# Kernel tuning notes

Hardware: AMD Instinct MI355X
Metric: run time of the kernel (lower is better)

The kernel has to match this reference:

```python
import jax, jax.numpy as jnp
import numpy as np

EMBED_DIM = 1024
NUM_HEADS = 16
HEAD_DIM = EMBED_DIM // NUM_HEADS


def setup_inputs() -> dict:
    key = jax.random.key(0)
    k_x, k_qkv, k_w, k_b = jax.random.split(key, 4)
    B, N, C = 2, 2048, EMBED_DIM
    scale = 1.0 / np.sqrt(C)
    x = jax.random.normal(k_x, (B, N, C), dtype=jnp.float32)
    # nn.Linear(embed_dim, 3*embed_dim, bias=False): weight [3C, C]
    w_qkv = jax.random.normal(k_qkv, (3 * C, C), dtype=jnp.float32) * scale
    # nn.Linear(embed_dim, embed_dim): weight [C, C], bias [C]
    w_out = jax.random.normal(k_w, (C, C), dtype=jnp.float32) * scale
    b_out = jax.random.normal(k_b, (C,), dtype=jnp.float32) * scale
    return {"x": x, "w_qkv": w_qkv, "w_out": w_out, "b_out": b_out}


def reference(x, w_qkv, w_out, b_out):
    B, N, C = x.shape
    H, D = NUM_HEADS, HEAD_DIM
    # qkv projection: [B,N,3C] -> [3,B,H,N,D]
    qkv = jnp.einsum("bnc,fc->bnf", x, w_qkv)
    qkv = qkv.reshape(B, N, 3, H, D).transpose(2, 0, 3, 1, 4)
    q, k, v = qkv[0], qkv[1], qkv[2]
    # scaled dot-product attention (dropout p=0 / eval mode -> identity)
    scores = jnp.einsum("bhnd,bhmd->bhnm", q, k) / np.sqrt(D).astype(x.dtype)
    attn = jax.nn.softmax(scores, axis=-1)
    out = jnp.einsum("bhnm,bhmd->bhnd", attn, v)
    out = out.transpose(0, 2, 1, 3).reshape(B, N, C)
    return jnp.einsum("bnc,oc->bno", out, w_out) + b_out
```

## Files before the change

### kernel.cpp

```cpp
#include <hip/hip_runtime.h>
#include <hip/hip_bf16.h>

typedef unsigned short u16;
typedef __attribute__((ext_vector_type(4))) float f32x4;
typedef __attribute__((ext_vector_type(8))) short bf16x8;

#define MFMA16(a, b, c) __builtin_amdgcn_mfma_f32_16x16x32_bf16(a, b, c, 0, 0, 0)

__device__ __forceinline__ u16 f2bf(float f) {
    union { float f; unsigned u; } v;
    v.f = f;
    unsigned r = v.u + 0x7FFFu + ((v.u >> 16) & 1u);
    return (u16)(r >> 16);
}

__device__ __forceinline__ int4 pack8(const float4 a, const float4 b) {
    int4 r;
    r.x = (int)((unsigned)f2bf(a.x) | ((unsigned)f2bf(a.y) << 16));
    r.y = (int)((unsigned)f2bf(a.z) | ((unsigned)f2bf(a.w) << 16));
    r.z = (int)((unsigned)f2bf(b.x) | ((unsigned)f2bf(b.y) << 16));
    r.w = (int)((unsigned)f2bf(b.z) | ((unsigned)f2bf(b.w) << 16));
    return r;
}

__device__ __forceinline__ unsigned pk2(float a, float b) {
    __hip_bfloat162 t = __float22bfloat162_rn(make_float2(a, b));
    union { __hip_bfloat162 h; unsigned u; } c;
    c.h = t;
    return c.u;
}

__device__ __forceinline__ void gload_lds16(const u16* g, u16* l) {
    __builtin_amdgcn_global_load_lds(
        (const __attribute__((address_space(1))) void*)g,
        (__attribute__((address_space(3))) void*)l, 16, 0, 0);
}

__global__ __launch_bounds__(256) void cvt_kernel(
    const float* __restrict__ x, const float* __restrict__ wq,
    const float* __restrict__ wo, u16* __restrict__ outb)
{
    size_t i = ((size_t)blockIdx.x * 256 + threadIdx.x) * 8;
    const float* src;
    size_t off;
    if (i < 4194304)      { src = x;  off = i; }
    else if (i < 7340032) { src = wq; off = i - 4194304; }
    else                  { src = wo; off = i - 7340032; }
    float4 a = *(const float4*)(src + off);
    float4 b = *(const float4*)(src + off + 4);
    *(int4*)(outb + i) = pack8(a, b);
}

__global__ __launch_bounds__(512) void qkv_gemm_kernel(
    const u16* __restrict__ X, const u16* __restrict__ W,
    u16* __restrict__ qws, u16* __restrict__ kws, u16* __restrict__ vws)
{
    __shared__ __align__(16) u16 Ash[256 * 64];
    __shared__ __align__(16) u16 Bsh[128 * 64];
    const int id = blockIdx.x;
    const int xcd = id & 7, slot = id >> 3;
    const int bm = (xcd >> 1) * 4 + (slot & 3);
    const int bn = (xcd & 1) * 12 + (slot >> 2);
    const int tid = threadIdx.x;
    const int lane = tid & 63, wid = tid >> 6;
    const int wm = wid >> 1, wn = wid & 1;
    const int g = lane >> 4, lq = lane & 15;

    f32x4 acc[4][4];
#pragma unroll
    for (int i = 0; i < 4; i++)
#pragma unroll
        for (int j = 0; j < 4; j++) acc[i][j] = (f32x4){0.f, 0.f, 0.f, 0.f};

    const int lrow = lane >> 3;
    const int lchunk = (lane & 7) ^ lrow;
    const u16* Ab = X + (size_t)(bm * 256 + lrow) * 1024 + lchunk * 8;
    const u16* Bb = W + (size_t)(bn * 128 + lrow) * 1024 + lchunk * 8;

    for (int kt = 0; kt < 16; ++kt) {
#pragma unroll
        for (int i = 0; i < 4; i++) {
            int sub = wid * 4 + i;
            gload_lds16(Ab + (size_t)sub * 8192 + kt * 64, &Ash[sub * 512]);
        }
#pragma unroll
        for (int i = 0; i < 2; i++) {
            int sub = wid * 2 + i;
            gload_lds16(Bb + (size_t)sub * 8192 + kt * 64, &Bsh[sub * 512]);
        }
        __syncthreads();
#pragma unroll
        for (int ka = 0; ka < 2; ka++) {
            bf16x8 af[4], bfr[4];
#pragma unroll
            for (int mt = 0; mt < 4; mt++) {
                int row = wm * 64 + mt * 16 + lq;
                af[mt] = *(const bf16x8*)&Ash[row * 64 + (((ka * 4 + g) ^ (row & 7)) << 3)];
            }
#pragma unroll
            for (int nt = 0; nt < 4; nt++) {
                int row = wn * 64 + nt * 16 + lq;
                bfr[nt] = *(const bf16x8*)&Bsh[row * 64 + (((ka * 4 + g) ^ (row & 7)) << 3)];
            }
#pragma unroll
            for (int mt = 0; mt < 4; mt++)
#pragma unroll
                for (int nt = 0; nt < 4; nt++)
                    acc[mt][nt] = MFMA16(af[mt], bfr[nt], acc[mt][nt]);
        }
        __syncthreads();
    }

#pragma unroll
    for (int mt = 0; mt < 4; mt++) {
#pragma unroll
        for (int nt = 0; nt < 4; nt++) {
            int f = bn * 128 + wn * 64 + nt * 16 + lq;
            int t = f >> 10, h = (f >> 6) & 15, d = f & 63;
            int mbase = bm * 256 + wm * 64 + mt * 16 + g * 4;
            int b = mbase >> 11, n0 = mbase & 2047;
            if (t == 0) {
#pragma unroll
                for (int r = 0; r < 4; r++)
                    qws[((size_t)(b * 16 + h) * 2048 + n0 + r) * 64 + d] =
                        f2bf(acc[mt][nt][r] * 0.18033688f);
            } else if (t == 1) {
#pragma unroll
                for (int r = 0; r < 4; r++)
                    kws[((size_t)(b * 16 + h) * 2048 + n0 + r) * 64 + d] =
                        f2bf(acc[mt][nt][r]);
            } else {
                ushort4 pk;
                pk.x = f2bf(acc[mt][nt][0]);
                pk.y = f2bf(acc[mt][nt][1]);
                pk.z = f2bf(acc[mt][nt][2]);
                pk.w = f2bf(acc[mt][nt][3]);
                *(ushort4*)&vws[((size_t)(b * 16 + h) * 64 + d) * 2048 + n0] = pk;
            }
        }
    }
}

__global__ __launch_bounds__(256, 2) void attn_kernel(
    const u16* __restrict__ qws, const u16* __restrict__ kws,
    const u16* __restrict__ vws, float* __restrict__ Opart,
    float* __restrict__ lpart)
{
    __shared__ __align__(16) u16 Ksh[2][64 * 64];
    __shared__ __align__(16) u16 Vsh[2][64 * 64];
    __shared__ __align__(16) u16 Psh[4][64 * 64];
    const int bh = blockIdx.x, qt = blockIdx.y, kvh = blockIdx.z;
    const int tid = threadIdx.x, wid = tid >> 6, lane = tid & 63;
    const int g = lane >> 4, lq = lane & 15;

    const u16* Qp = qws + ((size_t)bh * 2048 + qt * 256 + wid * 64) * 64;
    bf16x8 qf[4][2];
#pragma unroll
    for (int qa = 0; qa < 4; qa++) {
        qf[qa][0] = *(const bf16x8*)(Qp + (qa * 16 + lq) * 64 + g * 8);
        qf[qa][1] = *(const bf16x8*)(Qp + (qa * 16 + lq) * 64 + 32 + g * 8);
    }

    const int lrow = lane >> 3;
    const int lchunk = (lane & 7) ^ lrow;
    const u16* Kb = kws + (size_t)bh * 2048 * 64 + (size_t)lrow * 64 + lchunk * 8;
    const u16* Vb = vws + (size_t)bh * 64 * 2048 + (size_t)lrow * 2048 + lchunk * 8;

#define STAGE(TG, BUF)                                                        \
    {                                                                         \
        _Pragma("unroll")                                                     \
        for (int i = 0; i < 2; i++) {                                         \
            int sub = wid * 2 + i;                                            \
            gload_lds16(Kb + (size_t)((TG) * 64 + sub * 8) * 64,              \
                        &Ksh[BUF][sub * 512]);                                \
            gload_lds16(Vb + (size_t)(sub * 8) * 2048 + (TG) * 64,            \
                        &Vsh[BUF][sub * 512]);                                \
        }                                                                     \
    }

    bf16x8 onesB;
#pragma unroll
    for (int i = 0; i < 8; i++) onesB[i] = (short)0x3F80;

    f32x4 oacc[4][4];
#pragma unroll
    for (int qa = 0; qa < 4; qa++)
#pragma unroll
        for (int i = 0; i < 4; i++) oacc[qa][i] = (f32x4){0.f, 0.f, 0.f, 0.f};
    f32x4 lacc[4];
#pragma unroll
    for (int qa = 0; qa < 4; qa++) lacc[qa] = (f32x4){0.f, 0.f, 0.f, 0.f};

    const int tbase = kvh * 16;
    STAGE(tbase, 0);

    for (int t = 0; t < 16; ++t) {
        const int buf = t & 1;
        STAGE(tbase + ((t + 1) & 15), buf ^ 1);
        asm volatile("s_waitcnt vmcnt(4)" ::: "memory");
        __builtin_amdgcn_s_barrier();
        __builtin_amdgcn_sched_barrier(0);

#pragma unroll
        for (int nt = 0; nt < 4; nt++) {
            int row = nt * 16 + lq;
            bf16x8 kb0 = *(const bf16x8*)&Ksh[buf][row * 64 + ((g ^ (row & 7)) << 3)];
            bf16x8 kb1 = *(const bf16x8*)&Ksh[buf][row * 64 + (((4 + g) ^ (row & 7)) << 3)];
            int c16 = nt * 2 + (g >> 1);
#pragma unroll
            for (int qa = 0; qa < 4; qa++) {
                f32x4 z = (f32x4){0.f, 0.f, 0.f, 0.f};
                z = MFMA16(kb0, qf[qa][0], z);
                z = MFMA16(kb1, qf[qa][1], z);
#pragma unroll
                for (int r = 0; r < 4; r++) z[r] = __builtin_amdgcn_exp2f(z[r]);
                uint2 pk;
                pk.x = pk2(z[0], z[1]);
                pk.y = pk2(z[2], z[3]);
                int prow = qa * 16 + lq;
                *(uint2*)&Psh[wid][prow * 64 + (((c16 ^ (lq & 7)) << 3) | ((g & 1) << 2))] = pk;
            }
        }
        asm volatile("s_waitcnt lgkmcnt(0)" ::: "memory");
        __builtin_amdgcn_sched_barrier(0);

        __builtin_amdgcn_s_setprio(1);
#pragma unroll
        for (int qp = 0; qp < 2; qp++) {
            bf16x8 pa[2][2];
#pragma unroll
            for (int q2 = 0; q2 < 2; q2++) {
                int prow = (qp * 2 + q2) * 16 + lq;
                pa[q2][0] = *(const bf16x8*)&Psh[wid][prow * 64 + ((g ^ (lq & 7)) << 3)];
                pa[q2][1] = *(const bf16x8*)&Psh[wid][prow * 64 + (((4 + g) ^ (lq & 7)) << 3)];
                lacc[qp * 2 + q2] = MFMA16(pa[q2][0], onesB, lacc[qp * 2 + q2]);
                lacc[qp * 2 + q2] = MFMA16(pa[q2][1], onesB, lacc[qp * 2 + q2]);
            }
#pragma unroll
            for (int dt = 0; dt < 4; dt++) {
                int vrow = dt * 16 + lq;
                bf16x8 vb0 = *(const bf16x8*)&Vsh[buf][vrow * 64 + ((g ^ (vrow & 7)) << 3)];
                bf16x8 vb1 = *(const bf16x8*)&Vsh[buf][vrow * 64 + (((4 + g) ^ (vrow & 7)) << 3)];
#pragma unroll
                for (int q2 = 0; q2 < 2; q2++) {
                    oacc[qp * 2 + q2][dt] = MFMA16(pa[q2][0], vb0, oacc[qp * 2 + q2][dt]);
                    oacc[qp * 2 + q2][dt] = MFMA16(pa[q2][1], vb1, oacc[qp * 2 + q2][dt]);
                }
            }
        }
        __builtin_amdgcn_s_setprio(0);
        asm volatile("s_waitcnt lgkmcnt(0)" ::: "memory");
        __builtin_amdgcn_s_barrier();
    }
#undef STAGE

    const int nbase = qt * 256 + wid * 64;
#pragma unroll
    for (int qa = 0; qa < 4; qa++) {
#pragma unroll
        for (int dt = 0; dt < 4; dt++)
#pragma unroll
            for (int r = 0; r < 4; r++) {
                int n = nbase + qa * 16 + g * 4 + r;
                Opart[(size_t)kvh * 4194304 + ((size_t)bh * 2048 + n) * 64 + dt * 16 + lq] =
                    oacc[qa][dt][r];
            }
        if (lq == 0) {
#pragma unroll
            for (int r = 0; r < 4; r++)
                lpart[kvh * 65536 + bh * 2048 + nbase + qa * 16 + g * 4 + r] =
                    lacc[qa][r];
        }
    }
}

__global__ __launch_bounds__(256) void combine_kernel(
    const float* __restrict__ Opart, const float* __restrict__ lpart,
    u16* __restrict__ ows)
{
    int idx = blockIdx.x * 256 + threadIdx.x;
    int d4 = (idx & 15) * 4;
    int n  = (idx >> 4) & 2047;
    int bh = idx >> 15;
    size_t o = ((size_t)bh * 2048 + n) * 64 + d4;
    float4 a = *(const float4*)(Opart + o);
    float4 c = *(const float4*)(Opart + 4194304 + o);
    float rl = 1.0f / (lpart[bh * 2048 + n] + lpart[65536 + bh * 2048 + n]);
    ushort4 pk;
    pk.x = f2bf((a.x + c.x) * rl);
    pk.y = f2bf((a.y + c.y) * rl);
    pk.z = f2bf((a.z + c.z) * rl);
    pk.w = f2bf((a.w + c.w) * rl);
    int b = bh >> 4, h = bh & 15;
    *(ushort4*)&ows[((size_t)b * 2048 + n) * 1024 + h * 64 + d4] = pk;
}

__global__ __launch_bounds__(256) void out_gemm_kernel(
    const u16* __restrict__ A, const u16* __restrict__ W,
    const float* __restrict__ bias, float* __restrict__ Out)
{
    __shared__ __align__(16) u16 Ash[128 * 64];
    __shared__ __align__(16) u16 Bsh[128 * 64];
    const int id = blockIdx.x;
    const int xcd = id & 7, slot = id >> 3;
    const int bm = (xcd >> 1) * 8 + (slot & 7);
    const int bn = (xcd & 1) * 4 + (slot >> 3);
    const int tid = threadIdx.x;
    const int lane = tid & 63, wid = tid >> 6;
    const int wm = wid >> 1, wn = wid & 1;
    const int g = lane >> 4, lq = lane & 15;

    f32x4 acc[4][4];
#pragma unroll
    for (int i = 0; i < 4; i++)
#pragma unroll
        for (int j = 0; j < 4; j++) acc[i][j] = (f32x4){0.f, 0.f, 0.f, 0.f};

    const int lrow = lane >> 3;
    const int lchunk = (lane & 7) ^ lrow;
    const u16* Ab = A + (size_t)(bm * 128 + lrow) * 1024 + lchunk * 8;
    const u16* Bb = W + (size_t)(bn * 128 + lrow) * 1024 + lchunk * 8;

    for (int kt = 0; kt < 16; ++kt) {
#pragma unroll
        for (int i = 0; i < 4; i++) {
            int sub = i * 4 + wid;
            gload_lds16(Ab + (size_t)sub * 8192 + kt * 64, &Ash[sub * 512]);
            gload_lds16(Bb + (size_t)sub * 8192 + kt * 64, &Bsh[sub * 512]);
        }
        __syncthreads();
#pragma unroll
        for (int ka = 0; ka < 2; ka++) {
            bf16x8 af[4], bfr[4];
#pragma unroll
            for (int mt = 0; mt < 4; mt++) {
                int row = wm * 64 + mt * 16 + lq;
                af[mt] = *(const bf16x8*)&Ash[row * 64 + (((ka * 4 + g) ^ (row & 7)) << 3)];
            }
#pragma unroll
            for (int nt = 0; nt < 4; nt++) {
                int row = wn * 64 + nt * 16 + lq;
                bfr[nt] = *(const bf16x8*)&Bsh[row * 64 + (((ka * 4 + g) ^ (row & 7)) << 3)];
            }
#pragma unroll
            for (int mt = 0; mt < 4; mt++)
#pragma unroll
                for (int nt = 0; nt < 4; nt++)
                    acc[mt][nt] = MFMA16(af[mt], bfr[nt], acc[mt][nt]);
        }
        __syncthreads();
    }

#pragma unroll
    for (int mt = 0; mt < 4; mt++) {
#pragma unroll
        for (int nt = 0; nt < 4; nt++) {
            int ncol = bn * 128 + wn * 64 + nt * 16 + lq;
            float bv = bias[ncol];
            int mbase = bm * 128 + wm * 64 + mt * 16 + g * 4;
#pragma unroll
            for (int r = 0; r < 4; r++)
                Out[(size_t)(mbase + r) * 1024 + ncol] = acc[mt][nt][r] + bv;
        }
    }
}

extern "C" void kernel_launch(void* const* d_in, const int* in_sizes, int n_in,
                              void* d_out, int out_size, void* d_ws, size_t ws_size,
                              hipStream_t stream) {
    const float* x     = (const float*)d_in[0];
    const float* w_qkv = (const float*)d_in[1];
    const float* w_out = (const float*)d_in[2];
    const float* b_out = (const float*)d_in[3];
    float* out = (float*)d_out;

    u16* xb  = (u16*)d_ws;
    u16* wqb = xb + 4194304;
    u16* wob = wqb + 3145728;
    u16* qws = wob + 1048576;
    u16* kws = qws + 4194304;
    u16* vws = kws + 4194304;
    u16* ows = vws + 4194304;
    float* Opart = (float*)(ows + 4194304);
    float* lpart = Opart + 8388608;

    cvt_kernel<<<4096, 256, 0, stream>>>(x, w_qkv, w_out, xb);
    qkv_gemm_kernel<<<384, 512, 0, stream>>>(xb, wqb, qws, kws, vws);
    attn_kernel<<<dim3(32, 8, 2), 256, 0, stream>>>(qws, kws, vws, Opart, lpart);
    combine_kernel<<<4096, 256, 0, stream>>>(Opart, lpart, ows);
    out_gemm_kernel<<<256, 256, 0, stream>>>(ows, wob, b_out, out);
}
```

Before: 113.6 us.

## Keep attention probabilities in registers and enlarge output GEMM tiles

The attention kernel stops writing exp'd scores to shared memory and reading them back. It instead permutes the K rows so that the QK^T MFMA output layout lines up directly with the A-operand layout of the PV MFMA, and packs the P fragments in registers. This removes the Psh buffer, its LDS writes and reads, and one waitcnt. The K/V staging uses a new rotation-based swizzle to match. Separately, the output projection GEMM moves to 512-thread blocks with 256x128 tiles and half as many blocks, which raises reuse of the B operand but leaves fewer blocks per CU.

```diff
diff --git a/kernel.cpp b/kernel.cpp
--- a/kernel.cpp
+++ b/kernel.cpp
@@ -28,6 +28,15 @@
     union { __hip_bfloat162 h; unsigned u; } c;
     c.h = t;
     return c.u;
+}
+
+__device__ __forceinline__ bf16x8 mk_pa(f32x4 a, f32x4 b) {
+    union { uint4 u; bf16x8 v; } r;
+    r.u.x = pk2(a[0], a[1]);
+    r.u.y = pk2(a[2], a[3]);
+    r.u.z = pk2(b[0], b[1]);
+    r.u.w = pk2(b[2], b[3]);
+    return r.v;
 }
 
 __device__ __forceinline__ void gload_lds16(const u16* g, u16* l) {
@@ -148,7 +157,6 @@
 {
     __shared__ __align__(16) u16 Ksh[2][64 * 64];
     __shared__ __align__(16) u16 Vsh[2][64 * 64];
-    __shared__ __align__(16) u16 Psh[4][64 * 64];
     const int bh = blockIdx.x, qt = blockIdx.y, kvh = blockIdx.z;
     const int tid = threadIdx.x, wid = tid >> 6, lane = tid & 63;
     const int g = lane >> 4, lq = lane & 15;
@@ -161,21 +169,37 @@
         qf[qa][1] = *(const bf16x8*)(Qp + (qa * 16 + lq) * 64 + 32 + g * 8);
     }
 
-    const int lrow = lane >> 3;
-    const int lchunk = (lane & 7) ^ lrow;
-    const u16* Kb = kws + (size_t)bh * 2048 * 64 + (size_t)lrow * 64 + lchunk * 8;
-    const u16* Vb = vws + (size_t)bh * 64 * 2048 + (size_t)lrow * 2048 + lchunk * 8;
+    const int lr8 = lane >> 3;
+    const int c0 = ((lane & 7) - lr8) & 7;
+    const u16* Kb = kws + (size_t)bh * 2048 * 64;
+    const u16* Vb = vws + (size_t)bh * 64 * 2048;
 
 #define STAGE(TG, BUF)                                                        \
     {                                                                         \
         _Pragma("unroll")                                                     \
         for (int i = 0; i < 2; i++) {                                         \
             int sub = wid * 2 + i;                                            \
-            gload_lds16(Kb + (size_t)((TG) * 64 + sub * 8) * 64,              \
+            int c = (c0 - 2 * sub) & 7;                                       \
+            gload_lds16(Kb + (size_t)((TG) * 64 + sub * 8 + lr8) * 64 + c * 8,\
                         &Ksh[BUF][sub * 512]);                                \
-            gload_lds16(Vb + (size_t)(sub * 8) * 2048 + (TG) * 64,            \
+            gload_lds16(Vb + (size_t)(sub * 8 + lr8) * 2048 + (TG) * 64 + c * 8,\
                         &Vsh[BUF][sub * 512]);                                \
         }                                                                     \
+    }
+
+    int koff[4][2];
+#pragma unroll
+    for (int j = 0; j < 4; j++) {
+        int R = (j >> 1) * 32 + (lq >> 2) * 8 + (j & 1) * 4 + (lq & 3);
+        koff[j][0] = R * 64 + (((g)     + (R & 7) + 2 * (R >> 3)) & 7) * 8;
+        koff[j][1] = R * 64 + (((4 + g) + (R & 7) + 2 * (R >> 3)) & 7) * 8;
+    }
+    int voff[4][2];
+#pragma unroll
+    for (int dt = 0; dt < 4; dt++) {
+        int vr = dt * 16 + lq;
+        voff[dt][0] = vr * 64 + (((g)     + (vr & 7) + 2 * (vr >> 3)) & 7) * 8;
+        voff[dt][1] = vr * 64 + (((4 + g) + (vr & 7) + 2 * (vr >> 3)) & 7) * 8;
     }
 
     bf16x8 onesB;
@@ -201,55 +225,85 @@
         __builtin_amdgcn_s_barrier();
         __builtin_amdgcn_sched_barrier(0);
 
-#pragma unroll
-        for (int nt = 0; nt < 4; nt++) {
-            int row = nt * 16 + lq;
-            bf16x8 kb0 = *(const bf16x8*)&Ksh[buf][row * 64 + ((g ^ (row & 7)) << 3)];
-            bf16x8 kb1 = *(const bf16x8*)&Ksh[buf][row * 64 + (((4 + g) ^ (row & 7)) << 3)];
-            int c16 = nt * 2 + (g >> 1);
+        const u16* Kt = Ksh[buf];
+        const u16* Vt = Vsh[buf];
+
+        bf16x8 pa0[4], pa1[4];
+        {
+            f32x4 za[4], zb[4];
+            bf16x8 k0 = *(const bf16x8*)&Kt[koff[0][0]];
+            bf16x8 k1 = *(const bf16x8*)&Kt[koff[0][1]];
 #pragma unroll
             for (int qa = 0; qa < 4; qa++) {
                 f32x4 z = (f32x4){0.f, 0.f, 0.f, 0.f};
-                z = MFMA16(kb0, qf[qa][0], z);
-                z = MFMA16(kb1, qf[qa][1], z);
-#pragma unroll
-                for (int r = 0; r < 4; r++) z[r] = __builtin_amdgcn_exp2f(z[r]);
-                uint2 pk;
-                pk.x = pk2(z[0], z[1]);
-                pk.y = pk2(z[2], z[3]);
-                int prow = qa * 16 + lq;
-                *(uint2*)&Psh[wid][prow * 64 + (((c16 ^ (lq & 7)) << 3) | ((g & 1) << 2))] = pk;
-            }
-        }
-        asm volatile("s_waitcnt lgkmcnt(0)" ::: "memory");
-        __builtin_amdgcn_sched_barrier(0);
+                z = MFMA16(k0, qf[qa][0], z);
+                z = MFMA16(k1, qf[qa][1], z);
+                za[qa] = z;
+            }
+            k0 = *(const bf16x8*)&Kt[koff[1][0]];
+            k1 = *(const bf16x8*)&Kt[koff[1][1]];
+#pragma unroll
+            for (int qa = 0; qa < 4; qa++) {
+                f32x4 z = (f32x4){0.f, 0.f, 0.f, 0.f};
+                z = MFMA16(k0, qf[qa][0], z);
+                z = MFMA16(k1, qf[qa][1], z);
+                zb[qa] = z;
+            }
+#pragma unroll
+            for (int qa = 0; qa < 4; qa++) {
+#pragma unroll
+                for (int r = 0; r < 4; r++) {
+                    za[qa][r] = __builtin_amdgcn_exp2f(za[qa][r]);
+                    zb[qa][r] = __builtin_amdgcn_exp2f(zb[qa][r]);
+                }
+                pa0[qa] = mk_pa(za[qa], zb[qa]);
+            }
+            k0 = *(const bf16x8*)&Kt[koff[2][0]];
+            k1 = *(const bf16x8*)&Kt[koff[2][1]];
+#pragma unroll
+            for (int qa = 0; qa < 4; qa++) {
+                f32x4 z = (f32x4){0.f, 0.f, 0.f, 0.f};
+                z = MFMA16(k0, qf[qa][0], z);
+                z = MFMA16(k1, qf[qa][1], z);
+                za[qa] = z;
+            }
+            k0 = *(const bf16x8*)&Kt[koff[3][0]];
+            k1 = *(const bf16x8*)&Kt[koff[3][1]];
+#pragma unroll
+            for (int qa = 0; qa < 4; qa++) {
+                f32x4 z = (f32x4){0.f, 0.f, 0.f, 0.f};
+                z = MFMA16(k0, qf[qa][0], z);
+                z = MFMA16(k1, qf[qa][1], z);
+                zb[qa] = z;
+            }
+#pragma unroll
+            for (int qa = 0; qa < 4; qa++) {
+#pragma unroll
+                for (int r = 0; r < 4; r++) {
+                    za[qa][r] = __builtin_amdgcn_exp2f(za[qa][r]);
+                    zb[qa][r] = __builtin_amdgcn_exp2f(zb[qa][r]);
+                }
+                pa1[qa] = mk_pa(za[qa], zb[qa]);
+            }
+        }
 
         __builtin_amdgcn_s_setprio(1);
 #pragma unroll
-        for (int qp = 0; qp < 2; qp++) {
-            bf16x8 pa[2][2];
-#pragma unroll
-            for (int q2 = 0; q2 < 2; q2++) {
-                int prow = (qp * 2 + q2) * 16 + lq;
-                pa[q2][0] = *(const bf16x8*)&Psh[wid][prow * 64 + ((g ^ (lq & 7)) << 3)];
-                pa[q2][1] = *(const bf16x8*)&Psh[wid][prow * 64 + (((4 + g) ^ (lq & 7)) << 3)];
-                lacc[qp * 2 + q2] = MFMA16(pa[q2][0], onesB, lacc[qp * 2 + q2]);
-                lacc[qp * 2 + q2] = MFMA16(pa[q2][1], onesB, lacc[qp * 2 + q2]);
-            }
-#pragma unroll
-            for (int dt = 0; dt < 4; dt++) {
-                int vrow = dt * 16 + lq;
-                bf16x8 vb0 = *(const bf16x8*)&Vsh[buf][vrow * 64 + ((g ^ (vrow & 7)) << 3)];
-                bf16x8 vb1 = *(const bf16x8*)&Vsh[buf][vrow * 64 + (((4 + g) ^ (vrow & 7)) << 3)];
-#pragma unroll
-                for (int q2 = 0; q2 < 2; q2++) {
-                    oacc[qp * 2 + q2][dt] = MFMA16(pa[q2][0], vb0, oacc[qp * 2 + q2][dt]);
-                    oacc[qp * 2 + q2][dt] = MFMA16(pa[q2][1], vb1, oacc[qp * 2 + q2][dt]);
-                }
+        for (int qa = 0; qa < 4; qa++) {
+            lacc[qa] = MFMA16(pa0[qa], onesB, lacc[qa]);
+            lacc[qa] = MFMA16(pa1[qa], onesB, lacc[qa]);
+        }
+#pragma unroll
+        for (int dt = 0; dt < 4; dt++) {
+            bf16x8 vb0 = *(const bf16x8*)&Vt[voff[dt][0]];
+            bf16x8 vb1 = *(const bf16x8*)&Vt[voff[dt][1]];
+#pragma unroll
+            for (int qa = 0; qa < 4; qa++) {
+                oacc[qa][dt] = MFMA16(pa0[qa], vb0, oacc[qa][dt]);
+                oacc[qa][dt] = MFMA16(pa1[qa], vb1, oacc[qa][dt]);
             }
         }
         __builtin_amdgcn_s_setprio(0);
-        asm volatile("s_waitcnt lgkmcnt(0)" ::: "memory");
         __builtin_amdgcn_s_barrier();
     }
 #undef STAGE
@@ -295,16 +349,16 @@
     *(ushort4*)&ows[((size_t)b * 2048 + n) * 1024 + h * 64 + d4] = pk;
 }
 
-__global__ __launch_bounds__(256) void out_gemm_kernel(
+__global__ __launch_bounds__(512) void out_gemm_kernel(
     const u16* __restrict__ A, const u16* __restrict__ W,
     const float* __restrict__ bias, float* __restrict__ Out)
 {
-    __shared__ __align__(16) u16 Ash[128 * 64];
+    __shared__ __align__(16) u16 Ash[256 * 64];
     __shared__ __align__(16) u16 Bsh[128 * 64];
     const int id = blockIdx.x;
     const int xcd = id & 7, slot = id >> 3;
-    const int bm = (xcd >> 1) * 8 + (slot & 7);
-    const int bn = (xcd & 1) * 4 + (slot >> 3);
+    const int bm = xcd * 2 + (slot & 1);
+    const int bn = slot >> 1;
     const int tid = threadIdx.x;
     const int lane = tid & 63, wid = tid >> 6;
     const int wm = wid >> 1, wn = wid & 1;
@@ -318,14 +372,18 @@
 
     const int lrow = lane >> 3;
     const int lchunk = (lane & 7) ^ lrow;
-    const u16* Ab = A + (size_t)(bm * 128 + lrow) * 1024 + lchunk * 8;
+    const u16* Ab = A + (size_t)(bm * 256 + lrow) * 1024 + lchunk * 8;
     const u16* Bb = W + (size_t)(bn * 128 + lrow) * 1024 + lchunk * 8;
 
     for (int kt = 0; kt < 16; ++kt) {
 #pragma unroll
         for (int i = 0; i < 4; i++) {
-            int sub = i * 4 + wid;
+            int sub = wid * 4 + i;
             gload_lds16(Ab + (size_t)sub * 8192 + kt * 64, &Ash[sub * 512]);
+        }
+#pragma unroll
+        for (int i = 0; i < 2; i++) {
+            int sub = wid * 2 + i;
             gload_lds16(Bb + (size_t)sub * 8192 + kt * 64, &Bsh[sub * 512]);
         }
         __syncthreads();
@@ -357,7 +415,7 @@
         for (int nt = 0; nt < 4; nt++) {
             int ncol = bn * 128 + wn * 64 + nt * 16 + lq;
             float bv = bias[ncol];
-            int mbase = bm * 128 + wm * 64 + mt * 16 + g * 4;
+            int mbase = bm * 256 + wm * 64 + mt * 16 + g * 4;
 #pragma unroll
             for (int r = 0; r < 4; r++)
                 Out[(size_t)(mbase + r) * 1024 + ncol] = acc[mt][nt][r] + bv;
@@ -388,5 +446,5 @@
     qkv_gemm_kernel<<<384, 512, 0, stream>>>(xb, wqb, qws, kws, vws);
     attn_kernel<<<dim3(32, 8, 2), 256, 0, stream>>>(qws, kws, vws, Opart, lpart);
     combine_kernel<<<4096, 256, 0, stream>>>(Opart, lpart, ows);
-    out_gemm_kernel<<<256, 256, 0, stream>>>(ows, wob, b_out, out);
-}
+    out_gemm_kernel<<<128, 512, 0, stream>>>(ows, wob, b_out, out);
+}
```

Result: slower. 116.5 us (+2.5%).
